# Kernel tuning notes

Measured on AMD Instinct MI355X. Metric: run time of the kernel, lower is better.

Reference implementation:

```python
import jax, jax.numpy as jnp
import numpy as np

B, T, I, H, K, C, TH, CLS = 128, 512, 300, 150, 6, 300, 20, 5

def setup_inputs() -> dict:
    key = jax.random.key(0)
    ks = jax.random.split(key, 16)
    s = lambda *sh: 1.0 / np.sqrt(sh[-1])
    inp = {
        "x": jax.random.normal(ks[0], (B, T, I), jnp.float32),
        # GRU params (PyTorch layout: [3H, in]) for fwd/bwd directions
        "Wih_f": jax.random.normal(ks[1], (3 * H, I), jnp.float32) * s(3 * H, I),
        "Whh_f": jax.random.normal(ks[2], (3 * H, H), jnp.float32) * s(3 * H, H),
        "bih_f": jax.random.normal(ks[3], (3 * H,), jnp.float32) * 0.01,
        "bhh_f": jax.random.normal(ks[4], (3 * H,), jnp.float32) * 0.01,
        "Wih_b": jax.random.normal(ks[5], (3 * H, I), jnp.float32) * s(3 * H, I),
        "Whh_b": jax.random.normal(ks[6], (3 * H, H), jnp.float32) * s(3 * H, H),
        "bih_b": jax.random.normal(ks[7], (3 * H,), jnp.float32) * 0.01,
        "bhh_b": jax.random.normal(ks[8], (3 * H,), jnp.float32) * 0.01,
        # topic attention params (stacked over K topics)
        "attn_context": jax.random.normal(ks[9], (K, C), jnp.float32),
        "Wattn": jax.random.normal(ks[10], (K, C + 2 * H, 2 * H), jnp.float32) * s(1, C + 2 * H),
        "battn": jax.random.normal(ks[11], (K, 2 * H), jnp.float32) * 0.01,
        "Wtop": jax.random.normal(ks[12], (K, 2 * H, TH), jnp.float32) * s(1, 2 * H),
        "btop": jax.random.normal(ks[13], (K, TH), jnp.float32) * 0.01,
        "Wout": jax.random.normal(ks[14], (K * TH, CLS), jnp.float32) * s(1, K * TH),
        "bout": jax.random.normal(ks[15], (CLS,), jnp.float32) * 0.01,
    }
    return inp

def _gru_dir(x, Wih, Whh, bih, bhh, reverse):
    # x: [B,T,I] -> outputs [B,T,H], final hidden [B,H]
    xT = jnp.swapaxes(x, 0, 1)                    # [T,B,I]
    if reverse:
        xT = xT[::-1]
    gi = xT @ Wih.T + bih                         # [T,B,3H] input projections (one big GEMM)
    h0 = jnp.zeros((x.shape[0], Whh.shape[1]), x.dtype)
    def step(h, g):
        gh = h @ Whh.T + bhh
        i_r, i_z, i_n = jnp.split(g, 3, axis=-1)
        h_r, h_z, h_n = jnp.split(gh, 3, axis=-1)
        r = jax.nn.sigmoid(i_r + h_r)
        z = jax.nn.sigmoid(i_z + h_z)
        n = jnp.tanh(i_n + r * h_n)
        h_new = (1.0 - z) * n + z * h
        return h_new, h_new
    hT, ys = jax.lax.scan(step, h0, gi)
    if reverse:
        ys = ys[::-1]
    return jnp.swapaxes(ys, 0, 1), hT

def reference(x, Wih_f, Whh_f, bih_f, bhh_f, Wih_b, Whh_b, bih_b, bhh_b,
              attn_context, Wattn, battn, Wtop, btop, Wout, bout):
    # eval mode: dropout is identity
    out_f, h_f = _gru_dir(x, Wih_f, Whh_f, bih_f, bhh_f, False)
    out_b, h_b = _gru_dir(x, Wih_b, Whh_b, bih_b, bhh_b, True)
    seq = jnp.concatenate([out_f, out_b], axis=-1)       # [B,T,2H]
    hidden = jnp.concatenate([h_f, h_b], axis=-1)        # [B,2H]
    Bsz = x.shape[0]
    Kt = attn_context.shape[0]
    # per-topic context: cat(context_k, hidden) -> linear -> tanh, batched over topics
    ctx_in = jnp.concatenate([
        jnp.broadcast_to(attn_context[None, :, :], (Bsz, Kt, attn_context.shape[1])),
        jnp.broadcast_to(hidden[:, None, :], (Bsz, Kt, hidden.shape[1])),
    ], axis=-1)                                          # [B,K,C+2H]
    context = jnp.tanh(jnp.einsum('bkc,kcd->bkd', ctx_in, Wattn) + battn)  # [B,K,2H]
    # attention pooling over time, all topics at once
    energy = jnp.einsum('btd,bkd->btk', seq, context)    # [B,T,K]
    probs = jax.nn.softmax(energy, axis=1)
    pooled = jnp.einsum('btd,btk->bkd', seq, probs)      # [B,K,2H]
    topic = jax.nn.relu(jnp.einsum('bkd,kdh->bkh', pooled, Wtop) + btop)   # [B,K,TH]
    feats = topic.reshape(Bsz, -1)                       # [B,K*TH]
    logits = feats @ Wout + bout
    out = jax.nn.softmax(logits, axis=1)                 # eval + validate=False path
    # regularization loss on normalized contexts
    nc = context / jnp.linalg.norm(context, axis=2, keepdims=True).clip(1e-12)
    G = jnp.einsum('bkd,bjd->bkj', nc, nc)               # [B,K,K]
    diff = G - jnp.eye(Kt, dtype=G.dtype)[None]
    reg = jnp.mean(jnp.sqrt(jnp.sum(diff * diff, axis=(1, 2))))
    return out, reg
```

## Files before the change

kernel.cpp:

```cpp
#include <hip/hip_runtime.h>
#include <hip/hip_bf16.h>
#include <math.h>

#define Bq   128
#define Tq   512
#define Iq   300
#define Hq   150
#define G3   450
#define Kq   6
#define Cq   300
#define D2   300
#define THq  20
#define CLSq 5

typedef __attribute__((ext_vector_type(8))) short short8;
typedef __attribute__((ext_vector_type(4))) float floatx4;

__global__ __launch_bounds__(256) void cast_bf16_kernel(
    const float* __restrict__ in, __hip_bfloat16* __restrict__ out, int n4)
{
    const int i = blockIdx.x * 256 + threadIdx.x;
    if (i < n4) {
        float4 v = *(const float4*)(in + 4 * (size_t)i);
        out[4 * (size_t)i + 0] = __float2bfloat16(v.x);
        out[4 * (size_t)i + 1] = __float2bfloat16(v.y);
        out[4 * (size_t)i + 2] = __float2bfloat16(v.z);
        out[4 * (size_t)i + 3] = __float2bfloat16(v.w);
    }
}

#define LB 40

__global__ __launch_bounds__(256) void gi_gemm_mfma(
    const __hip_bfloat16* __restrict__ xb,
    const __hip_bfloat16* __restrict__ Wbf,
    const float* __restrict__ bf_, const float* __restrict__ bb_,
    float* __restrict__ gic, int t0f, int t0b, int tcShift)
{
    const int dir = blockIdx.z;
    const unsigned short* W = (const unsigned short*)(Wbf + (size_t)dir * G3 * Iq);
    const unsigned short* X = (const unsigned short*)xb;
    const float* bias = dir ? bb_ : bf_;
    const int t0 = dir ? t0b : t0f;
    const int TCr = 1 << tcShift;
    float* outb = gic + (size_t)dir * Bq * TCr * G3;

    const int m0 = blockIdx.y * 128;
    const int n0 = blockIdx.x * 128;
    const int tid  = threadIdx.x;
    const int wv   = tid >> 6, lane = tid & 63;
    const int wm   = wv & 1,  wn   = wv >> 1;
    const int quad = lane >> 4, mr = lane & 15;

    __shared__ __align__(16) unsigned short Ab[128 * LB];
    __shared__ __align__(16) unsigned short Bb[128 * LB];

    floatx4 acc[4][4];
    #pragma unroll
    for (int i = 0; i < 4; ++i)
        #pragma unroll
        for (int j = 0; j < 4; ++j)
            acc[i][j] = (floatx4){0.f, 0.f, 0.f, 0.f};

    for (int k0 = 0; k0 < 320; k0 += 32) {
        __syncthreads();
        #pragma unroll
        for (int i = 0; i < 4; ++i) {
            const int g = tid + 256 * i;
            const int row = g >> 3, kq = g & 7;
            const int k = k0 + kq * 4;
            const int r = m0 + row;
            const int bb2 = r >> tcShift, lt = r & (TCr - 1);
            ushort4 av = make_ushort4(0, 0, 0, 0);
            if (k < Iq)
                av = *(const ushort4*)(X + ((size_t)bb2 * Tq + t0 + lt) * Iq + k);
            *(ushort4*)&Ab[row * LB + kq * 4] = av;
            const int n = n0 + row;
            ushort4 bv = make_ushort4(0, 0, 0, 0);
            if (n < G3 && k < Iq)
                bv = *(const ushort4*)(W + (size_t)n * Iq + k);
            *(ushort4*)&Bb[row * LB + kq * 4] = bv;
        }
        __syncthreads();

        short8 af[4], bfr[4];
        #pragma unroll
        for (int i = 0; i < 4; ++i)
            af[i] = *(const short8*)&Ab[(wm * 64 + i * 16 + mr) * LB + quad * 8];
        #pragma unroll
        for (int j = 0; j < 4; ++j)
            bfr[j] = *(const short8*)&Bb[(wn * 64 + j * 16 + mr) * LB + quad * 8];
        #pragma unroll
        for (int i = 0; i < 4; ++i)
            #pragma unroll
            for (int j = 0; j < 4; ++j)
                acc[i][j] = __builtin_amdgcn_mfma_f32_16x16x32_bf16(
                    af[i], bfr[j], acc[i][j], 0, 0, 0);
    }

    #pragma unroll
    for (int j = 0; j < 4; ++j) {
        const int gn = n0 + wn * 64 + j * 16 + mr;
        if (gn >= G3) continue;
        const float bv = bias[gn];
        #pragma unroll
        for (int i = 0; i < 4; ++i) {
            const int mbase = m0 + wm * 64 + i * 16 + quad * 4;
            #pragma unroll
            for (int rg = 0; rg < 4; ++rg)
                outb[(size_t)(mbase + rg) * G3 + gn] = acc[i][j][rg] + bv;
        }
    }
}

__global__ __launch_bounds__(512, 2) void gru_rec(
    const float* __restrict__ gic,
    const float* __restrict__ Whh_f, const float* __restrict__ bhh_f,
    const float* __restrict__ Whh_b, const float* __restrict__ bhh_b,
    float* __restrict__ hstate,
    float* __restrict__ seq,
    int chunk, int tcShift)
{
    const int TCr = 1 << tcShift;
    const int bid = blockIdx.x;
    const int dir = bid & 1;
    const int b   = bid >> 1;
    const float* Whh = dir ? Whh_b : Whh_f;
    const float* bhh = dir ? bhh_b : bhh_f;
    const int tid = threadIdx.x;
    const int rq  = tid >> 2;
    const int p   = tid & 3;
    const bool gact = (rq < 113);
    const bool iact = (tid < 450);

    __shared__ __align__(16) float stage[64 * 150];
    __shared__ __align__(16) float4 hbuf4[40];
    __shared__ __align__(16) float ghp[4][456];
    __shared__ float gi_s[456];
    float* hbuf = (float*)hbuf4;

    float w[4][40];

    for (int c = 0; c < 8; ++c) {
        const int r0 = c * 64;
        const int nrows = (r0 + 64 <= G3) ? 64 : (G3 - r0);
        const int nel = nrows * 150;
        __syncthreads();
        for (int idx = tid * 4; idx < nel; idx += 512 * 4)
            *(float4*)&stage[idx] = *(const float4*)(Whh + (size_t)r0 * 150 + idx);
        __syncthreads();
        if (gact && (rq >> 4) == c) {
            const int rl = 4 * rq - r0;
            const int cmax = (p == 3) ? 36 : 38;
            #pragma unroll
            for (int r = 0; r < 4; ++r) {
                const bool rv = (4 * rq + r < G3);
                #pragma unroll
                for (int cc = 0; cc < 40; ++cc)
                    w[r][cc] = (rv && cc < cmax)
                             ? stage[(rl + r) * 150 + p * 38 + cc] : 0.f;
            }
        }
    }

    float bh3[3] = {0.f, 0.f, 0.f};
    if (tid < Hq) {
        bh3[0] = bhh[tid];
        bh3[1] = bhh[150 + tid];
        bh3[2] = bhh[300 + tid];
    }
    const int hslot = (tid / 38) * 40 + (tid % 38);

    float* hs = hstate + (size_t)(dir * Bq + b) * Hq;
    if (tid < 160) {
        const int pp = tid / 40, off = tid % 40;
        const int j = pp * 38 + off;
        hbuf[tid] = (off < 38 && j < Hq && chunk > 0) ? hs[j] : 0.f;
    }
    __syncthreads();

    const float* gib = gic + (size_t)(dir * Bq + b) * TCr * G3;
    const int t0 = dir ? (Tq - TCr * (chunk + 1)) : (chunk * TCr);
    float* seqb = seq + (size_t)b * Tq * D2 + dir * Hq;

    int lt = dir ? (TCr - 1) : 0;
    float gval = iact ? gib[(size_t)lt * G3 + tid] : 0.f;

    for (int s = 0; s < TCr; ++s) {
        const int ltn = dir ? (TCr - 2 - s) : (s + 1);
        float gnext = 0.f;
        if (s + 1 < TCr && iact)
            gnext = gib[(size_t)ltn * G3 + tid];

        if (iact) gi_s[tid] = gval;

        if (gact) {
            const float4* hh = hbuf4 + p * 10;
            float acc0 = 0.f, acc1 = 0.f, acc2 = 0.f, acc3 = 0.f;
            #pragma unroll
            for (int q = 0; q < 10; ++q) {
                const float4 hv = hh[q];
                acc0 += hv.x * w[0][4*q]   + hv.y * w[0][4*q+1]
                      + hv.z * w[0][4*q+2] + hv.w * w[0][4*q+3];
                acc1 += hv.x * w[1][4*q]   + hv.y * w[1][4*q+1]
                      + hv.z * w[1][4*q+2] + hv.w * w[1][4*q+3];
                acc2 += hv.x * w[2][4*q]   + hv.y * w[2][4*q+1]
                      + hv.z * w[2][4*q+2] + hv.w * w[2][4*q+3];
                acc3 += hv.x * w[3][4*q]   + hv.y * w[3][4*q+1]
                      + hv.z * w[3][4*q+2] + hv.w * w[3][4*q+3];
            }
            *(float4*)&ghp[p][4 * rq] = make_float4(acc0, acc1, acc2, acc3);
        }
        __syncthreads();

        if (tid < Hq) {
            const float ghr = ghp[0][tid] + ghp[1][tid]
                            + ghp[2][tid] + ghp[3][tid] + bh3[0];
            const float ghz = ghp[0][150+tid] + ghp[1][150+tid]
                            + ghp[2][150+tid] + ghp[3][150+tid] + bh3[1];
            const float ghn = ghp[0][300+tid] + ghp[1][300+tid]
                            + ghp[2][300+tid] + ghp[3][300+tid] + bh3[2];
            const float r = 1.f / (1.f + __expf(-(gi_s[tid]       + ghr)));
            const float z = 1.f / (1.f + __expf(-(gi_s[150 + tid] + ghz)));
            const float nv = tanhf(gi_s[300 + tid] + r * ghn);
            const float hn = (1.f - z) * nv + z * hbuf[hslot];
            hbuf[hslot] = hn;
            stage[(s & 63) * 150 + tid] = hn;
        }
        __syncthreads();

        if ((s & 63) == 63 || s == TCr - 1) {
            const int sf0 = s & ~63;
            const int nf2 = (s - sf0 + 1) * 75;
            for (int idx = tid; idx < nf2; idx += 512) {
                const int rrow = idx / 75, cc = idx % 75;
                const int ss = sf0 + rrow;
                const int ltw = dir ? (TCr - 1 - ss) : ss;
                *(float2*)(seqb + (size_t)(t0 + ltw) * D2 + 2 * cc) =
                    *(const float2*)&stage[rrow * 150 + 2 * cc];
            }
        }

        gval = gnext;
        lt = ltn;
    }

    if (tid < Hq) hs[tid] = hbuf[hslot];
}

__global__ void ctxw_kernel(
    const float* __restrict__ attn_context,
    const float* __restrict__ Wattn,
    const float* __restrict__ battn,
    float* __restrict__ ctxW)
{
    const int o = blockIdx.x * 256 + threadIdx.x;
    if (o >= Kq * D2) return;
    const int k = o / D2, d = o % D2;
    float acc = battn[o];
    const float* Wp = Wattn + ((size_t)k * (Cq + D2)) * D2 + d;
    for (int c = 0; c < Cq; ++c)
        acc += attn_context[k * Cq + c] * Wp[(size_t)c * D2];
    ctxW[o] = acc;
}

__global__ __launch_bounds__(256) void ctx_compute(
    const float* __restrict__ seq,
    const float* __restrict__ Wattn,
    const float* __restrict__ ctxW,
    float* __restrict__ context,
    float* __restrict__ normsq)
{
    const int b = blockIdx.x;
    const int k = blockIdx.y;
    const int tid = threadIdx.x;
    const int lane = tid & 63, wv = tid >> 6;

    __shared__ float hb[304];
    __shared__ float red[4];

    for (int i = tid; i < D2; i += 256)
        hb[i] = (i < Hq) ? seq[((size_t)b * Tq + (Tq - 1)) * D2 + i]
                         : seq[(size_t)b * Tq * D2 + i];
    __syncthreads();

    float ssq = 0.f;
    for (int d = tid; d < D2; d += 256) {
        float acc = ctxW[k * D2 + d];
        const float* Wp = Wattn + ((size_t)k * (Cq + D2) + Cq) * D2 + d;
        for (int jj = 0; jj < D2; ++jj)
            acc += hb[jj] * Wp[(size_t)jj * D2];
        const float c = tanhf(acc);
        context[((size_t)b * Kq + k) * D2 + d] = c;
        ssq += c * c;
    }
    for (int off = 32; off > 0; off >>= 1) ssq += __shfl_xor(ssq, off, 64);
    if (lane == 0) red[wv] = ssq;
    __syncthreads();
    if (tid == 0) normsq[b * Kq + k] = red[0] + red[1] + red[2] + red[3];
}

__global__ __launch_bounds__(256) void gram_kernel(
    const float* __restrict__ context,
    const float* __restrict__ normsq,
    float* __restrict__ regbuf)
{
    const int b = blockIdx.x;
    const int tid = threadIdx.x;
    __shared__ float ctx[Kq * D2];
    __shared__ float Gm[36];

    for (int o = tid; o < Kq * D2; o += 256)
        ctx[o] = context[(size_t)b * Kq * D2 + o];
    __syncthreads();

    if (tid < 36) {
        const int k = tid / 6, jj = tid % 6;
        float g = 0.f;
        for (int d = 0; d < D2; ++d)
            g += ctx[k * D2 + d] * ctx[jj * D2 + d];
        const float nk = fmaxf(sqrtf(normsq[b * Kq + k]), 1e-12f);
        const float nj = fmaxf(sqrtf(normsq[b * Kq + jj]), 1e-12f);
        g /= (nk * nj);
        const float diff = g - ((k == jj) ? 1.f : 0.f);
        Gm[tid] = diff * diff;
    }
    __syncthreads();
    if (tid == 0) {
        float s = 0.f;
        for (int i = 0; i < 36; ++i) s += Gm[i];
        regbuf[b] = sqrtf(s);
    }
}

__global__ __launch_bounds__(256) void energy_kernel(
    const float* __restrict__ seq,
    const float* __restrict__ context,
    float* __restrict__ en)
{
    const int tc = blockIdx.x;
    const int b  = blockIdx.y;
    const int tid = threadIdx.x;
    const int lane = tid & 63, wv = tid >> 6;

    __shared__ float ctx[Kq * D2];
    for (int o = tid; o < Kq * D2; o += 256)
        ctx[o] = context[(size_t)b * Kq * D2 + o];
    __syncthreads();

    const float* seqb = seq + (size_t)b * Tq * D2;
    for (int s = 0; s < 16; ++s) {
        const int tt = tc * 64 + s * 4 + wv;
        float acc[Kq] = {0.f,0.f,0.f,0.f,0.f,0.f};
        for (int d = lane; d < D2; d += 64) {
            const float sv = seqb[(size_t)tt * D2 + d];
            #pragma unroll
            for (int k = 0; k < Kq; ++k) acc[k] += sv * ctx[k * D2 + d];
        }
        #pragma unroll
        for (int k = 0; k < Kq; ++k) {
            float v = acc[k];
            for (int off = 32; off > 0; off >>= 1) v += __shfl_xor(v, off, 64);
            if (lane == 0) en[((size_t)b * Tq + tt) * Kq + k] = v;
        }
    }
}

__global__ __launch_bounds__(256) void softmax_kernel(float* __restrict__ en)
{
    const int b = blockIdx.x;
    const int tid = threadIdx.x;
    const int lane = tid & 63, wv = tid >> 6;
    __shared__ float es[Tq * Kq];
    __shared__ float red[8];

    for (int o = tid; o < Tq * Kq; o += 256)
        es[o] = en[(size_t)b * Tq * Kq + o];
    __syncthreads();

    for (int k = 0; k < Kq; ++k) {
        float m = -1e30f;
        for (int tt = tid; tt < Tq; tt += 256) m = fmaxf(m, es[tt * Kq + k]);
        for (int off = 32; off > 0; off >>= 1) m = fmaxf(m, __shfl_xor(m, off, 64));
        if (lane == 0) red[wv] = m;
        __syncthreads();
        m = fmaxf(fmaxf(red[0], red[1]), fmaxf(red[2], red[3]));
        float ssum = 0.f;
        for (int tt = tid; tt < Tq; tt += 256) {
            const float e = __expf(es[tt * Kq + k] - m);
            es[tt * Kq + k] = e;
            ssum += e;
        }
        for (int off = 32; off > 0; off >>= 1) ssum += __shfl_xor(ssum, off, 64);
        if (lane == 0) red[4 + wv] = ssum;
        __syncthreads();
        const float inv = 1.f / (red[4] + red[5] + red[6] + red[7]);
        for (int tt = tid; tt < Tq; tt += 256) es[tt * Kq + k] *= inv;
        __syncthreads();
    }

    for (int o = tid; o < Tq * Kq; o += 256)
        en[(size_t)b * Tq * Kq + o] = es[o];
}

__global__ __launch_bounds__(256) void pooledp_kernel(
    const float* __restrict__ seq,
    const float* __restrict__ en,
    float* __restrict__ partial)
{
    const int tc = blockIdx.x;
    const int b  = blockIdx.y;
    const int tid = threadIdx.x;
    const int lane = tid & 63, wv = tid >> 6;

    __shared__ float pr[64 * Kq];
    __shared__ float part[4][Kq * D2];

    if (tid < 64 * Kq / 2) {
        pr[tid]       = en[((size_t)b * Tq + tc * 64) * Kq + tid];
        pr[tid + 192] = en[((size_t)b * Tq + tc * 64) * Kq + tid + 192];
    }
    __syncthreads();

    const float* seqb = seq + (size_t)b * Tq * D2;

    float pp[Kq][5];
    #pragma unroll
    for (int k = 0; k < Kq; ++k)
        #pragma unroll
        for (int q = 0; q < 5; ++q) pp[k][q] = 0.f;

    for (int s = 0; s < 16; ++s) {
        const int tl = s * 4 + wv;
        const int tt = tc * 64 + tl;
        float prr[Kq];
        #pragma unroll
        for (int k = 0; k < Kq; ++k) prr[k] = pr[tl * Kq + k];
        #pragma unroll
        for (int q = 0; q < 5; ++q) {
            const int d = lane + q * 64;
            const float sv = (d < D2) ? seqb[(size_t)tt * D2 + d] : 0.f;
            #pragma unroll
            for (int k = 0; k < Kq; ++k) pp[k][q] += prr[k] * sv;
        }
    }
    #pragma unroll
    for (int k = 0; k < Kq; ++k)
        #pragma unroll
        for (int q = 0; q < 5; ++q) {
            const int d = lane + q * 64;
            if (d < D2) part[wv][k * D2 + d] = pp[k][q];
        }
    __syncthreads();
    float* op = partial + ((size_t)b * 8 + tc) * (Kq * D2);
    for (int o = tid; o < Kq * D2; o += 256)
        op[o] = part[0][o] + part[1][o] + part[2][o] + part[3][o];
}

__global__ __launch_bounds__(256) void final_kernel(
    const float* __restrict__ partial,
    const float* __restrict__ Wtop,
    const float* __restrict__ btop,
    const float* __restrict__ Wout,
    const float* __restrict__ bout,
    float* __restrict__ outp)
{
    const int b = blockIdx.x;
    const int tid = threadIdx.x;
    __shared__ float pooled[Kq * D2];
    __shared__ float feats[Kq * THq];
    __shared__ float lsm[8];

    for (int o = tid; o < Kq * D2; o += 256) {
        float s = 0.f;
        #pragma unroll
        for (int c = 0; c < 8; ++c)
            s += partial[((size_t)b * 8 + c) * (Kq * D2) + o];
        pooled[o] = s;
    }
    __syncthreads();

    if (tid < Kq * THq) {
        const int k = tid / THq, hh = tid % THq;
        float acc = btop[tid];
        const float* wp = Wtop + (size_t)k * D2 * THq + hh;
        for (int d = 0; d < D2; ++d)
            acc += pooled[k * D2 + d] * wp[(size_t)d * THq];
        feats[tid] = fmaxf(acc, 0.f);
    }
    __syncthreads();

    if (tid < CLSq) {
        float acc = bout[tid];
        for (int f = 0; f < Kq * THq; ++f)
            acc += feats[f] * Wout[f * CLSq + tid];
        lsm[tid] = acc;
    }
    __syncthreads();
    if (tid < CLSq) {
        float m = lsm[0];
        for (int c = 1; c < CLSq; ++c) m = fmaxf(m, lsm[c]);
        float s = 0.f;
        for (int c = 0; c < CLSq; ++c) s += __expf(lsm[c] - m);
        outp[(size_t)b * CLSq + tid] = __expf(lsm[tid] - m) / s;
    }
}

__global__ void reg_final(const float* __restrict__ regbuf, float* __restrict__ outp)
{
    const int tid = threadIdx.x;
    float v = regbuf[tid];
    for (int off = 32; off > 0; off >>= 1) v += __shfl_xor(v, off, 64);
    __shared__ float r2[2];
    if ((tid & 63) == 0) r2[tid >> 6] = v;
    __syncthreads();
    if (tid == 0) outp[Bq * CLSq] = (r2[0] + r2[1]) * (1.f / (float)Bq);
}

extern "C" void kernel_launch(void* const* d_in, const int* in_sizes, int n_in,
                              void* d_out, int out_size, void* d_ws, size_t ws_size,
                              hipStream_t stream)
{
    const float* x     = (const float*)d_in[0];
    const float* Wih_f = (const float*)d_in[1];
    const float* Whh_f = (const float*)d_in[2];
    const float* bih_f = (const float*)d_in[3];
    const float* bhh_f = (const float*)d_in[4];
    const float* Wih_b = (const float*)d_in[5];
    const float* Whh_b = (const float*)d_in[6];
    const float* bih_b = (const float*)d_in[7];
    const float* bhh_b = (const float*)d_in[8];
    const float* attn_context = (const float*)d_in[9];
    const float* Wattn = (const float*)d_in[10];
    const float* battn = (const float*)d_in[11];
    const float* Wtop  = (const float*)d_in[12];
    const float* btop  = (const float*)d_in[13];
    const float* Wout  = (const float*)d_in[14];
    const float* bout  = (const float*)d_in[15];
    float* outp = (float*)d_out;

    float* ws       = (float*)d_ws;
    float* seqv     = ws;
    float* hstate   = seqv + (size_t)Bq * Tq * D2;
    float* ctxW     = hstate + (size_t)2 * Bq * Hq;
    float* context  = ctxW + Kq * D2;
    float* regbuf   = context + (size_t)Bq * Kq * D2;
    float* normsq   = regbuf + Bq;
    float* en       = normsq + Bq * Kq;
    float* partial  = en + (size_t)Bq * Tq * Kq;
    __hip_bfloat16* xb16 = (__hip_bfloat16*)(partial + (size_t)Bq * 8 * Kq * D2);
    __hip_bfloat16* Wb16 = xb16 + (size_t)Bq * Tq * Iq;
    float* gi_chunk = (float*)(Wb16 + (size_t)2 * G3 * Iq);
    const size_t fixed_floats = (size_t)(gi_chunk - ws);

    int tcShift = 5;
    for (int sh = 8; sh >= 5; --sh) {
        size_t need = (fixed_floats + (size_t)115200 * (1 << sh)) * 4;
        if (need <= ws_size) { tcShift = sh; break; }
    }
    const int TCr = 1 << tcShift;
    const int NL = Tq / TCr;

    cast_bf16_kernel<<<dim3((Bq * Tq * Iq / 4 + 255) / 256), 256, 0, stream>>>(
        x, xb16, Bq * Tq * Iq / 4);
    cast_bf16_kernel<<<dim3((G3 * Iq / 4 + 255) / 256), 256, 0, stream>>>(
        Wih_f, Wb16, G3 * Iq / 4);
    cast_bf16_kernel<<<dim3((G3 * Iq / 4 + 255) / 256), 256, 0, stream>>>(
        Wih_b, Wb16 + (size_t)G3 * Iq, G3 * Iq / 4);

    for (int c = 0; c < NL; ++c) {
        const int t0f = c * TCr;
        const int t0b = Tq - TCr * (c + 1);
        gi_gemm_mfma<<<dim3(4, Bq * TCr / 128, 2), 256, 0, stream>>>(
            xb16, Wb16, bih_f, bih_b, gi_chunk, t0f, t0b, tcShift);
        gru_rec<<<dim3(2 * Bq), 512, 0, stream>>>(
            gi_chunk, Whh_f, bhh_f, Whh_b, bhh_b, hstate, seqv, c, tcShift);
    }

    ctxw_kernel<<<dim3((Kq * D2 + 255) / 256), 256, 0, stream>>>(
        attn_context, Wattn, battn, ctxW);
    ctx_compute<<<dim3(Bq, Kq), 256, 0, stream>>>(seqv, Wattn, ctxW, context, normsq);
    gram_kernel<<<dim3(Bq), 256, 0, stream>>>(context, normsq, regbuf);
    energy_kernel<<<dim3(8, Bq), 256, 0, stream>>>(seqv, context, en);
    softmax_kernel<<<dim3(Bq), 256, 0, stream>>>(en);
    pooledp_kernel<<<dim3(8, Bq), 256, 0, stream>>>(seqv, en, partial);
    final_kernel<<<dim3(Bq), 256, 0, stream>>>(partial, Wtop, btop, Wout, bout, outp);
    reg_final<<<dim3(1), 128, 0, stream>>>(regbuf, outp);
}
```

Measured before the change: 1.053 ms.

## Reduce GRU recurrence partial sums with DPP and double-buffer hidden state

Restructures the recurrent step so each hidden unit is owned by a quad of four lanes. Each lane holds all three gate rows for a quarter of the columns, and the quad reduces its partial sums with DPP cross-lane adds. This removes the shared ghp/gi_s buffers and one of the two block barriers per timestep. The hidden state is double-buffered in shared memory and also kept in a register. The block grows from 512 to 640 threads with three 40-float weight arrays per lane, which may raise register pressure and reduce occupancy.

Result: slower. 1.296 ms (+23.1%).

```diff
diff --git a/kernel.cpp b/kernel.cpp
--- a/kernel.cpp
+++ b/kernel.cpp
@@ -113,7 +113,13 @@
     }
 }
 
-__global__ __launch_bounds__(512, 2) void gru_rec(
+template<int CTRL>
+__device__ __forceinline__ float qadd(float v) {
+    return v + __int_as_float(__builtin_amdgcn_update_dpp(
+        0, __float_as_int(v), CTRL, 0xF, 0xF, true));
+}
+
+__global__ __launch_bounds__(640) void gru_rec(
     const float* __restrict__ gic,
     const float* __restrict__ Whh_f, const float* __restrict__ bhh_f,
     const float* __restrict__ Whh_b, const float* __restrict__ bhh_b,
@@ -128,124 +134,111 @@
     const float* Whh = dir ? Whh_b : Whh_f;
     const float* bhh = dir ? bhh_b : bhh_f;
     const int tid = threadIdx.x;
-    const int rq  = tid >> 2;
+    const int t   = tid >> 2;
     const int p   = tid & 3;
-    const bool gact = (rq < 113);
-    const bool iact = (tid < 450);
+    const bool act = (t < Hq);
 
     __shared__ __align__(16) float stage[64 * 150];
-    __shared__ __align__(16) float4 hbuf4[40];
-    __shared__ __align__(16) float ghp[4][456];
-    __shared__ float gi_s[456];
-    float* hbuf = (float*)hbuf4;
-
-    float w[4][40];
-
-    for (int c = 0; c < 8; ++c) {
-        const int r0 = c * 64;
-        const int nrows = (r0 + 64 <= G3) ? 64 : (G3 - r0);
-        const int nel = nrows * 150;
-        __syncthreads();
-        for (int idx = tid * 4; idx < nel; idx += 512 * 4)
-            *(float4*)&stage[idx] = *(const float4*)(Whh + (size_t)r0 * 150 + idx);
-        __syncthreads();
-        if (gact && (rq >> 4) == c) {
-            const int rl = 4 * rq - r0;
-            const int cmax = (p == 3) ? 36 : 38;
-            #pragma unroll
-            for (int r = 0; r < 4; ++r) {
-                const bool rv = (4 * rq + r < G3);
-                #pragma unroll
-                for (int cc = 0; cc < 40; ++cc)
-                    w[r][cc] = (rv && cc < cmax)
-                             ? stage[(rl + r) * 150 + p * 38 + cc] : 0.f;
-            }
-        }
-    }
-
-    float bh3[3] = {0.f, 0.f, 0.f};
-    if (tid < Hq) {
-        bh3[0] = bhh[tid];
-        bh3[1] = bhh[150 + tid];
-        bh3[2] = bhh[300 + tid];
-    }
-    const int hslot = (tid / 38) * 40 + (tid % 38);
+    __shared__ __align__(16) float hbufs[2][160];
+
+    float w0[40], w1[40], w2[40];
+    const int c0 = p * 38;
+    const int cmax = (p == 3) ? 36 : 38;
+    if (act) {
+        #pragma unroll
+        for (int c = 0; c < 40; ++c) {
+            const bool v = (c < cmax);
+            const int col = c0 + (v ? c : 0);
+            w0[c] = v ? Whh[(size_t)t * Hq + col] : 0.f;
+            w1[c] = v ? Whh[(size_t)(Hq + t) * Hq + col] : 0.f;
+            w2[c] = v ? Whh[(size_t)(2 * Hq + t) * Hq + col] : 0.f;
+        }
+    }
+
+    float bhv = 0.f;
+    if (act && p < 3) bhv = bhh[p * Hq + t];
+    const int gidx = (p == 0) ? t : (p == 1) ? (Hq + t) : (2 * Hq + t);
+    const bool gload = act && (p != 2);
 
     float* hs = hstate + (size_t)(dir * Bq + b) * Hq;
-    if (tid < 160) {
-        const int pp = tid / 40, off = tid % 40;
+    float hprev = 0.f;
+    if (act && chunk > 0) hprev = hs[t];
+
+    if (tid < 320) {
+        const int buf = tid / 160, o = tid - buf * 160;
+        const int pp = o / 40, off = o % 40;
         const int j = pp * 38 + off;
-        hbuf[tid] = (off < 38 && j < Hq && chunk > 0) ? hs[j] : 0.f;
+        hbufs[buf][o] = (off < 38 && j < Hq && chunk > 0) ? hs[j] : 0.f;
     }
     __syncthreads();
 
     const float* gib = gic + (size_t)(dir * Bq + b) * TCr * G3;
     const int t0 = dir ? (Tq - TCr * (chunk + 1)) : (chunk * TCr);
     float* seqb = seq + (size_t)b * Tq * D2 + dir * Hq;
-
-    int lt = dir ? (TCr - 1) : 0;
-    float gval = iact ? gib[(size_t)lt * G3 + tid] : 0.f;
-
+    const int hslot = (t / 38) * 40 + (t % 38);
+
+    const int lt0 = dir ? (TCr - 1) : 0;
+    float gval = gload ? gib[(size_t)lt0 * G3 + gidx] : 0.f;
+
+    int cur = 0;
     for (int s = 0; s < TCr; ++s) {
         const int ltn = dir ? (TCr - 2 - s) : (s + 1);
         float gnext = 0.f;
-        if (s + 1 < TCr && iact)
-            gnext = gib[(size_t)ltn * G3 + tid];
-
-        if (iact) gi_s[tid] = gval;
-
-        if (gact) {
-            const float4* hh = hbuf4 + p * 10;
-            float acc0 = 0.f, acc1 = 0.f, acc2 = 0.f, acc3 = 0.f;
+        if (s + 1 < TCr && gload)
+            gnext = gib[(size_t)ltn * G3 + gidx];
+
+        if (act) {
+            const float base = bhv + gval;
+            float a0 = (p == 0) ? base : 0.f;
+            float a1 = (p == 1) ? base : 0.f;
+            float a2 = (p == 2) ? base : 0.f;
+            float a3 = (p == 3) ? base : 0.f;
+            const float4* hq = (const float4*)&hbufs[cur][p * 40];
             #pragma unroll
             for (int q = 0; q < 10; ++q) {
-                const float4 hv = hh[q];
-                acc0 += hv.x * w[0][4*q]   + hv.y * w[0][4*q+1]
-                      + hv.z * w[0][4*q+2] + hv.w * w[0][4*q+3];
-                acc1 += hv.x * w[1][4*q]   + hv.y * w[1][4*q+1]
-                      + hv.z * w[1][4*q+2] + hv.w * w[1][4*q+3];
-                acc2 += hv.x * w[2][4*q]   + hv.y * w[2][4*q+1]
-                      + hv.z * w[2][4*q+2] + hv.w * w[2][4*q+3];
-                acc3 += hv.x * w[3][4*q]   + hv.y * w[3][4*q+1]
-                      + hv.z * w[3][4*q+2] + hv.w * w[3][4*q+3];
+                const float4 hv = hq[q];
+                a0 += hv.x * w0[4*q]   + hv.y * w0[4*q+1]
+                    + hv.z * w0[4*q+2] + hv.w * w0[4*q+3];
+                a1 += hv.x * w1[4*q]   + hv.y * w1[4*q+1]
+                    + hv.z * w1[4*q+2] + hv.w * w1[4*q+3];
+                a2 += hv.x * w2[4*q]   + hv.y * w2[4*q+1]
+                    + hv.z * w2[4*q+2] + hv.w * w2[4*q+3];
             }
-            *(float4*)&ghp[p][4 * rq] = make_float4(acc0, acc1, acc2, acc3);
-        }
-        __syncthreads();
-
-        if (tid < Hq) {
-            const float ghr = ghp[0][tid] + ghp[1][tid]
-                            + ghp[2][tid] + ghp[3][tid] + bh3[0];
-            const float ghz = ghp[0][150+tid] + ghp[1][150+tid]
-                            + ghp[2][150+tid] + ghp[3][150+tid] + bh3[1];
-            const float ghn = ghp[0][300+tid] + ghp[1][300+tid]
-                            + ghp[2][300+tid] + ghp[3][300+tid] + bh3[2];
-            const float r = 1.f / (1.f + __expf(-(gi_s[tid]       + ghr)));
-            const float z = 1.f / (1.f + __expf(-(gi_s[150 + tid] + ghz)));
-            const float nv = tanhf(gi_s[300 + tid] + r * ghn);
-            const float hn = (1.f - z) * nv + z * hbuf[hslot];
-            hbuf[hslot] = hn;
-            stage[(s & 63) * 150 + tid] = hn;
+            a0 = qadd<0xB1>(a0); a1 = qadd<0xB1>(a1);
+            a2 = qadd<0xB1>(a2); a3 = qadd<0xB1>(a3);
+            a0 = qadd<0x4E>(a0); a1 = qadd<0x4E>(a1);
+            a2 = qadd<0x4E>(a2); a3 = qadd<0x4E>(a3);
+
+            const float r  = 1.f / (1.f + __expf(-a0));
+            const float z  = 1.f / (1.f + __expf(-a1));
+            const float nv = tanhf(a3 + r * a2);
+            const float hn = (1.f - z) * nv + z * hprev;
+            hprev = hn;
+            if (p == 0) {
+                hbufs[cur ^ 1][hslot] = hn;
+                stage[(s & 63) * 150 + t] = hn;
+            }
         }
         __syncthreads();
 
         if ((s & 63) == 63 || s == TCr - 1) {
             const int sf0 = s & ~63;
             const int nf2 = (s - sf0 + 1) * 75;
-            for (int idx = tid; idx < nf2; idx += 512) {
+            for (int idx = tid; idx < nf2; idx += 640) {
                 const int rrow = idx / 75, cc = idx % 75;
                 const int ss = sf0 + rrow;
                 const int ltw = dir ? (TCr - 1 - ss) : ss;
                 *(float2*)(seqb + (size_t)(t0 + ltw) * D2 + 2 * cc) =
                     *(const float2*)&stage[rrow * 150 + 2 * cc];
             }
+            __syncthreads();
         }
 
         gval = gnext;
-        lt = ltn;
-    }
-
-    if (tid < Hq) hs[tid] = hbuf[hslot];
+        cur ^= 1;
+    }
+
+    if (act && p == 0) hs[t] = hprev;
 }
 
 __global__ void ctxw_kernel(
@@ -573,7 +566,7 @@
         const int t0b = Tq - TCr * (c + 1);
         gi_gemm_mfma<<<dim3(4, Bq * TCr / 128, 2), 256, 0, stream>>>(
             xb16, Wb16, bih_f, bih_b, gi_chunk, t0f, t0b, tcShift);
-        gru_rec<<<dim3(2 * Bq), 512, 0, stream>>>(
+        gru_rec<<<dim3(2 * Bq), 640, 0, stream>>>(
             gi_chunk, Whh_f, bhh_f, Whh_b, bhh_b, hstate, seqv, c, tcShift);
     }
 
```
